# Performance work log

Hardware: AMD Instinct MI355X
Metric: run time of the kernel (lower is better)

The kernel has to match this reference:

```python
import jax, jax.numpy as jnp
import numpy as np

N_NODES = 100000


def gcn_conv(x, W, b, edge_index, n):
    """PyG-style GCNConv: x' = D^-1/2 (A+I) D^-1/2 (x W) + b."""
    loop = jnp.arange(n, dtype=edge_index.dtype)
    src = jnp.concatenate([edge_index[0], loop])
    dst = jnp.concatenate([edge_index[1], loop])
    deg = jax.ops.segment_sum(jnp.ones_like(dst, dtype=x.dtype), dst, num_segments=n)
    dinv = jax.lax.rsqrt(deg)  # deg >= 1 because of self-loops
    norm = dinv[src] * dinv[dst]  # [E+N]
    h = x @ W  # [N, out]
    msg = h[src] * norm[:, None]  # gather + scale
    return jax.ops.segment_sum(msg, dst, num_segments=n) + b


def edge_logits(z, edge_index, We, be):
    # concat(src_emb, dst_emb) @ We + be, without materializing the concat twice
    d = z.shape[1]
    return z[edge_index[0]] @ We[:d] + z[edge_index[1]] @ We[d:] + be


def setup_inputs() -> dict:
    key = jax.random.key(0)
    ks = jax.random.split(key, 10)
    x = jax.random.normal(ks[0], (N_NODES, 512), dtype=jnp.float32)
    edge_index = jax.random.randint(ks[1], (2, 3200000), 0, N_NODES, dtype=jnp.int64)
    pos_edge_index = jax.random.randint(ks[2], (2, 1000000), 0, N_NODES, dtype=jnp.int64)
    neg_edge_index = jax.random.randint(ks[3], (2, 1000000), 0, N_NODES, dtype=jnp.int64)
    s1 = 1.0 / np.sqrt(512)
    s2 = 1.0 / np.sqrt(16)
    se = 1.0 / np.sqrt(128)
    W1 = jax.random.uniform(ks[4], (512, 16), jnp.float32, -s1, s1)
    b1 = jnp.zeros((16,), jnp.float32)
    W2 = jax.random.uniform(ks[5], (16, 64), jnp.float32, -s2, s2)
    b2 = jnp.zeros((64,), jnp.float32)
    We = jax.random.uniform(ks[6], (128, 1), jnp.float32, -se, se)  # 2*num_classes -> 1
    be = jnp.zeros((1,), jnp.float32)
    return {"x": x, "W1": W1, "b1": b1, "W2": W2, "b2": b2, "We": We, "be": be,
            "edge_index": edge_index, "pos_edge_index": pos_edge_index,
            "neg_edge_index": neg_edge_index}


def reference(x, W1, b1, W2, b2, We, be, edge_index, pos_edge_index, neg_edge_index):
    n = x.shape[0]
    h = jax.nn.relu(gcn_conv(x, W1, b1, edge_index, n))
    z = gcn_conv(h, W2, b2, edge_index, n)  # node embeddings [N, num_classes]
    pos = edge_logits(z, pos_edge_index, We, be)
    neg = edge_logits(z, neg_edge_index, We, be)
    return z, jnp.concatenate([pos, neg], axis=0)
```

## Files before the change

kernel.cpp:

```cpp
#include <hip/hip_runtime.h>
#include <hip/hip_bf16.h>
#include <hip/hip_fp16.h>


constexpr int TPB = 256;
constexpr int LOG_W = 7;
constexpr int W_BKT = 128;
constexpr int NB_MAX = 1024;
constexpr int CAP = 5120;
constexpr int EPB = 8192;

__global__ __launch_bounds__(256) void scatterA_kernel(const int* __restrict__ src,
                                                       const int* __restrict__ dst,
                                                       int* __restrict__ bcursor,
                                                       int* __restrict__ pairs,
                                                       int E, int NB) {
    __shared__ int hist[NB_MAX];
    __shared__ int lstart[NB_MAX];
    __shared__ int gbase[NB_MAX];
    __shared__ int lcur[NB_MAX];
    __shared__ int csum[256];
    __shared__ int val[EPB];
    __shared__ unsigned short bkt[EPB];
    const int t = threadIdx.x;
    const int e0 = blockIdx.x * EPB;
    const int cnt = min(EPB, E - e0);

    for (int i = t; i < NB; i += 256) hist[i] = 0;
    __syncthreads();
    for (int i = t; i < cnt; i += 256) atomicAdd(&hist[dst[e0 + i] >> LOG_W], 1);
    __syncthreads();

    int loc[4], tsum = 0;
#pragma unroll
    for (int j = 0; j < 4; ++j) {
        int idx = t * 4 + j;
        int v = (idx < NB) ? hist[idx] : 0;
        loc[j] = tsum; tsum += v;
    }
    csum[t] = tsum;
    __syncthreads();
    for (int off = 1; off < 256; off <<= 1) {
        int v = (t >= off) ? csum[t - off] : 0;
        __syncthreads();
        csum[t] += v;
        __syncthreads();
    }
    int cbase = (t > 0) ? csum[t - 1] : 0;
#pragma unroll
    for (int j = 0; j < 4; ++j) {
        int idx = t * 4 + j;
        if (idx < NB) lstart[idx] = cbase + loc[j];
    }
    __syncthreads();
    for (int b = t; b < NB; b += 256) {
        gbase[b] = hist[b] ? atomicAdd(&bcursor[b], hist[b]) : 0;
        lcur[b] = lstart[b];
    }
    __syncthreads();
    for (int i = t; i < cnt; i += 256) {
        int s = src[e0 + i], d = dst[e0 + i];
        int b = d >> LOG_W;
        int p = atomicAdd(&lcur[b], 1);
        val[p] = ((d & (W_BKT - 1)) << 17) | s;
        bkt[p] = (unsigned short)b;
    }
    __syncthreads();
    for (int i = t; i < cnt; i += 256) {
        int b = bkt[i];
        int ofs = gbase[b] + (i - lstart[b]);
        if (ofs < CAP) pairs[(size_t)b * CAP + ofs] = val[i];
    }
}

__global__ __launch_bounds__(256) void bucketB_kernel(const int* __restrict__ bcursor,
                                                      int* __restrict__ pairs,
                                                      float* __restrict__ dinv,
                                                      int* __restrict__ row_start,
                                                      int* __restrict__ row_end,
                                                      int N) {
    __shared__ int cnt[W_BKT];
    __shared__ int scn[W_BKT];
    __shared__ int cur[W_BKT];
    __shared__ int img[CAP];
    const int b = blockIdx.x;
    const int t = threadIdx.x;
    const int len = min(bcursor[b], CAP);
    const int n0 = b * W_BKT;
    int* p = pairs + (size_t)b * CAP;

    if (t < W_BKT) cnt[t] = 0;
    __syncthreads();
    for (int i = t; i < len; i += 256) atomicAdd(&cnt[p[i] >> 17], 1);
    __syncthreads();
    if (t < W_BKT) scn[t] = cnt[t];
    __syncthreads();
    for (int off = 1; off < W_BKT; off <<= 1) {
        int v = (t < W_BKT && t >= off) ? scn[t - off] : 0;
        __syncthreads();
        if (t < W_BKT) scn[t] += v;
        __syncthreads();
    }
    if (t < W_BKT) {
        int c = cnt[t];
        int es = scn[t] - c;
        cur[t] = es;
        int n = n0 + t;
        if (n < N) {
            dinv[n] = rsqrtf((float)(c + 1));
            int rs = b * CAP + es;
            row_start[n] = rs;
            row_end[n] = rs + c;
        }
    }
    __syncthreads();
    for (int i = t; i < len; i += 256) {
        int v = p[i];
        int r = atomicAdd(&cur[v >> 17], 1);
        img[r] = v & 0x1FFFF;
    }
    __syncthreads();
    for (int i = t; i < len; i += 256) p[i] = img[i];
}

__global__ __launch_bounds__(256) void gemm1_kernel(const float* __restrict__ x,
                                                    const float* __restrict__ W1,
                                                    const float* __restrict__ dinv,
                                                    __half* __restrict__ xs, int N) {
    __shared__ float buf[512 * 16];
    const int t = threadIdx.x;
    {
        const float4* w4 = (const float4*)W1;
        float4* b4 = (float4*)buf;
        for (int i = t; i < 2048; i += 256) b4[i] = w4[i];
    }
    __syncthreads();

    const int r = t & 63, q = t >> 6;
    const int row = blockIdx.x * 64 + r;
    const bool valid = row < N;
    const float* xrow = x + (size_t)row * 512 + q * 128;

    float acc[16];
#pragma unroll
    for (int c = 0; c < 16; ++c) acc[c] = 0.0f;

    if (valid) {
        const int kb = q * 128;
#pragma unroll 2
        for (int k0 = 0; k0 < 128; k0 += 16) {
            const float4* xp = (const float4*)(xrow + k0);
            float4 a0 = xp[0], a1 = xp[1], a2 = xp[2], a3 = xp[3];
            float xv[16] = {a0.x, a0.y, a0.z, a0.w, a1.x, a1.y, a1.z, a1.w,
                            a2.x, a2.y, a2.z, a2.w, a3.x, a3.y, a3.z, a3.w};
#pragma unroll
            for (int kk = 0; kk < 16; ++kk) {
                const float4* wr = (const float4*)(buf + (kb + k0 + kk) * 16);
                float4 w0 = wr[0], w1 = wr[1], w2 = wr[2], w3 = wr[3];
                float xvk = xv[kk];
                acc[0]  += xvk * w0.x; acc[1]  += xvk * w0.y; acc[2]  += xvk * w0.z; acc[3]  += xvk * w0.w;
                acc[4]  += xvk * w1.x; acc[5]  += xvk * w1.y; acc[6]  += xvk * w1.z; acc[7]  += xvk * w1.w;
                acc[8]  += xvk * w2.x; acc[9]  += xvk * w2.y; acc[10] += xvk * w2.z; acc[11] += xvk * w2.w;
                acc[12] += xvk * w3.x; acc[13] += xvk * w3.y; acc[14] += xvk * w3.z; acc[15] += xvk * w3.w;
            }
        }
    }
    __syncthreads();

    float* red = buf;
    if (q > 0) {
        float4* d0 = (float4*)(red + ((q - 1) * 64 + r) * 16);
        d0[0] = make_float4(acc[0], acc[1], acc[2], acc[3]);
        d0[1] = make_float4(acc[4], acc[5], acc[6], acc[7]);
        d0[2] = make_float4(acc[8], acc[9], acc[10], acc[11]);
        d0[3] = make_float4(acc[12], acc[13], acc[14], acc[15]);
    }
    __syncthreads();
    if (q == 0 && valid) {
#pragma unroll
        for (int p = 0; p < 3; ++p) {
            const float* sr = red + (p * 64 + r) * 16;
#pragma unroll
            for (int c = 0; c < 16; ++c) acc[c] += sr[c];
        }
        float di = dinv[row];
        __half hv[16];
#pragma unroll
        for (int c = 0; c < 16; ++c) hv[c] = __float2half_rn(acc[c] * di);
        float4* o = (float4*)(xs + (size_t)row * 16);
        o[0] = *(const float4*)&hv[0];
        o[1] = *(const float4*)&hv[8];
    }
}

__global__ __launch_bounds__(256) void gather1_kernel(const __half* __restrict__ xs,
                                                      const int* __restrict__ csr,
                                                      const int* __restrict__ row_start,
                                                      const int* __restrict__ row_end,
                                                      const float* __restrict__ dinv,
                                                      const float* __restrict__ b1,
                                                      __half* __restrict__ hs, int N) {
    int t = threadIdx.x;
    int node = blockIdx.x * 16 + (t >> 4);
    int lane = t & 15;
    if (node >= N) return;
    int rs = row_start[node], re = row_end[node];
    float acc = __half2float(xs[(size_t)node * 16 + lane]);

    int e0 = rs;
    for (; e0 + 16 <= re; e0 += 16) {
        int idx = csr[e0 + lane];
        float v[16];
#pragma unroll
        for (int j = 0; j < 16; ++j) {
            int s = __shfl(idx, j, 16);
            v[j] = __half2float(xs[(size_t)s * 16 + lane]);
        }
#pragma unroll
        for (int j = 0; j < 16; ++j) acc += v[j];
    }
    if (e0 < re) {
        int idx = (e0 + lane < re) ? csr[e0 + lane] : 0;
        int m = re - e0;
        float v[16];
#pragma unroll
        for (int j = 0; j < 16; ++j) {
            int s = __shfl(idx, j, 16);
            v[j] = 0.0f;
            if (j < m) v[j] = __half2float(xs[(size_t)s * 16 + lane]);
        }
#pragma unroll
        for (int j = 0; j < 16; ++j) acc += v[j];
    }

    float di = dinv[node];
    float h = fmaxf(fmaf(di, acc, b1[lane]), 0.0f);
    hs[(size_t)node * 16 + lane] = __float2half_rn(h * di);
}

__global__ __launch_bounds__(256) void gather2_fin2_kernel(const __half* __restrict__ hs,
                                                           const int* __restrict__ csr,
                                                           const int* __restrict__ row_start,
                                                           const int* __restrict__ row_end,
                                                           const float* __restrict__ dinv,
                                                           const float* __restrict__ W2,
                                                           const float* __restrict__ b2,
                                                           const float* __restrict__ We,
                                                           float* __restrict__ z,
                                                           float* __restrict__ s1,
                                                           float* __restrict__ s2, int N) {
    __shared__ float w2l[16 * 64];
    __shared__ float wel[128];
    __shared__ float b2l[64];
    int t = threadIdx.x;
    for (int i = t; i < 1024; i += 256) w2l[i] = W2[i];
    if (t < 128) wel[t] = We[t];
    if (t < 64) b2l[t] = b2[t];
    __syncthreads();

    int g = t >> 4, lane = t & 15;
    int node = blockIdx.x * 16 + g;
    if (node >= N) return;

    int rs = row_start[node], re = row_end[node];
    float acc = __half2float(hs[(size_t)node * 16 + lane]);

    int e0 = rs;
    for (; e0 + 16 <= re; e0 += 16) {
        int idx = csr[e0 + lane];
        float v[16];
#pragma unroll
        for (int j = 0; j < 16; ++j) {
            int s = __shfl(idx, j, 16);
            v[j] = __half2float(hs[(size_t)s * 16 + lane]);
        }
#pragma unroll
        for (int j = 0; j < 16; ++j) acc += v[j];
    }
    if (e0 < re) {
        int idx = (e0 + lane < re) ? csr[e0 + lane] : 0;
        int m = re - e0;
        float v[16];
#pragma unroll
        for (int j = 0; j < 16; ++j) {
            int s = __shfl(idx, j, 16);
            v[j] = 0.0f;
            if (j < m) v[j] = __half2float(hs[(size_t)s * 16 + lane]);
        }
#pragma unroll
        for (int j = 0; j < 16; ++j) acc += v[j];
    }

    float uv = acc * dinv[node];

    int c0 = lane * 4;
    float z0 = b2l[c0], z1 = b2l[c0 + 1], z2 = b2l[c0 + 2], z3 = b2l[c0 + 3];
#pragma unroll
    for (int k = 0; k < 16; ++k) {
        float uk = __shfl(uv, k, 16);
        const float* wr = &w2l[k * 64 + c0];
        z0 = fmaf(uk, wr[0], z0);
        z1 = fmaf(uk, wr[1], z1);
        z2 = fmaf(uk, wr[2], z2);
        z3 = fmaf(uk, wr[3], z3);
    }
    float p1 = z0 * wel[c0] + z1 * wel[c0 + 1] + z2 * wel[c0 + 2] + z3 * wel[c0 + 3];
    float p2 = z0 * wel[64 + c0] + z1 * wel[64 + c0 + 1] + z2 * wel[64 + c0 + 2] + z3 * wel[64 + c0 + 3];
#pragma unroll
    for (int off = 1; off < 16; off <<= 1) {
        p1 += __shfl_xor(p1, off, 16);
        p2 += __shfl_xor(p2, off, 16);
    }
    ((float4*)(z + (size_t)node * 64))[lane] = make_float4(z0, z1, z2, z3);
    if (lane == 0) { s1[node] = p1; s2[node] = p2; }
}

__global__ void logits_kernel(const int* __restrict__ psrc, const int* __restrict__ pdst,
                              const int* __restrict__ nsrc, const int* __restrict__ ndst,
                              const float* __restrict__ s1, const float* __restrict__ s2,
                              const float* __restrict__ be, float* __restrict__ out,
                              int EP, int ET) {
    int e = blockIdx.x * blockDim.x + threadIdx.x;
    if (e >= ET) return;
    int s, d;
    if (e < EP) {
        s = psrc[e];
        d = pdst[e];
    } else {
        s = nsrc[e - EP];
        d = ndst[e - EP];
    }
    out[e] = s1[s] + s2[d] + be[0];
}

extern "C" void kernel_launch(void* const* d_in, const int* in_sizes, int n_in,
                              void* d_out, int out_size, void* d_ws, size_t ws_size,
                              hipStream_t stream) {
    const float* x  = (const float*)d_in[0];
    const float* W1 = (const float*)d_in[1];
    const float* b1 = (const float*)d_in[2];
    const float* W2 = (const float*)d_in[3];
    const float* b2 = (const float*)d_in[4];
    const float* We = (const float*)d_in[5];
    const float* be = (const float*)d_in[6];
    const int* ei   = (const int*)d_in[7];
    const int* pei  = (const int*)d_in[8];
    const int* nei  = (const int*)d_in[9];

    const int N  = in_sizes[0] / 512;
    const int E  = in_sizes[7] / 2;
    const int EP = in_sizes[8] / 2;
    const int EN = in_sizes[9] / 2;
    const int NB = (N + W_BKT - 1) >> LOG_W;

    const int* src  = ei;
    const int* dst  = ei + E;
    const int* psrc = pei;
    const int* pdst = pei + EP;
    const int* nsrc = nei;
    const int* ndst = nei + EN;

    int* wsp = (int*)d_ws;
    int*   bcursor   = wsp;
    float* dinv      = (float*)(wsp + NB_MAX);
    int*   row_start = (int*)(dinv + N);
    int*   row_end   = row_start + N;
    float* s1        = (float*)(row_end + N);
    float* s2        = s1 + N;
    __half* xs       = (__half*)(s2 + N);
    __half* hs       = xs + (size_t)16 * N;
    int*   pairs     = (int*)(hs + (size_t)16 * N);

    float* z_out = (float*)d_out;
    float* logit_out = z_out + (size_t)64 * N;

    hipMemsetAsync(bcursor, 0, NB_MAX * sizeof(int), stream);

    int gA  = (E + EPB - 1) / EPB;
    int g16 = (N + 15) / 16;
    int g64 = (N + 63) / 64;

    scatterA_kernel<<<gA, TPB, 0, stream>>>(src, dst, bcursor, pairs, E, NB);
    bucketB_kernel<<<NB, TPB, 0, stream>>>(bcursor, pairs, dinv, row_start, row_end, N);

    gemm1_kernel<<<g64, TPB, 0, stream>>>(x, W1, dinv, xs, N);

    gather1_kernel<<<g16, TPB, 0, stream>>>(xs, pairs, row_start, row_end, dinv, b1, hs, N);
    gather2_fin2_kernel<<<g16, TPB, 0, stream>>>(hs, pairs, row_start, row_end, dinv,
                                                 W2, b2, We, z_out, s1, s2, N);

    int ET = EP + EN;
    int gL = (ET + TPB - 1) / TPB;
    logits_kernel<<<gL, TPB, 0, stream>>>(psrc, pdst, nsrc, ndst, s1, s2, be,
                                          logit_out, EP, ET);
}
```

Baseline: 479.2 us.

## Replace per-node CSR gather with per-bucket edge-parallel LDS atomic accumulation

```diff
diff --git a/kernel.cpp b/kernel.cpp
--- a/kernel.cpp
+++ b/kernel.cpp
@@ -74,53 +74,23 @@
 }
 
 __global__ __launch_bounds__(256) void bucketB_kernel(const int* __restrict__ bcursor,
-                                                      int* __restrict__ pairs,
+                                                      const int* __restrict__ pairs,
                                                       float* __restrict__ dinv,
-                                                      int* __restrict__ row_start,
-                                                      int* __restrict__ row_end,
                                                       int N) {
     __shared__ int cnt[W_BKT];
-    __shared__ int scn[W_BKT];
-    __shared__ int cur[W_BKT];
-    __shared__ int img[CAP];
     const int b = blockIdx.x;
     const int t = threadIdx.x;
     const int len = min(bcursor[b], CAP);
-    const int n0 = b * W_BKT;
-    int* p = pairs + (size_t)b * CAP;
+    const int* p = pairs + (size_t)b * CAP;
 
     if (t < W_BKT) cnt[t] = 0;
     __syncthreads();
     for (int i = t; i < len; i += 256) atomicAdd(&cnt[p[i] >> 17], 1);
     __syncthreads();
-    if (t < W_BKT) scn[t] = cnt[t];
-    __syncthreads();
-    for (int off = 1; off < W_BKT; off <<= 1) {
-        int v = (t < W_BKT && t >= off) ? scn[t - off] : 0;
-        __syncthreads();
-        if (t < W_BKT) scn[t] += v;
-        __syncthreads();
-    }
     if (t < W_BKT) {
-        int c = cnt[t];
-        int es = scn[t] - c;
-        cur[t] = es;
-        int n = n0 + t;
-        if (n < N) {
-            dinv[n] = rsqrtf((float)(c + 1));
-            int rs = b * CAP + es;
-            row_start[n] = rs;
-            row_end[n] = rs + c;
-        }
-    }
-    __syncthreads();
-    for (int i = t; i < len; i += 256) {
-        int v = p[i];
-        int r = atomicAdd(&cur[v >> 17], 1);
-        img[r] = v & 0x1FFFF;
-    }
-    __syncthreads();
-    for (int i = t; i < len; i += 256) p[i] = img[i];
+        int n = b * W_BKT + t;
+        if (n < N) dinv[n] = rsqrtf((float)(cnt[t] + 1));
+    }
 }
 
 __global__ __launch_bounds__(256) void gemm1_kernel(const float* __restrict__ x,
@@ -193,126 +163,127 @@
     }
 }
 
-__global__ __launch_bounds__(256) void gather1_kernel(const __half* __restrict__ xs,
-                                                      const int* __restrict__ csr,
-                                                      const int* __restrict__ row_start,
-                                                      const int* __restrict__ row_end,
-                                                      const float* __restrict__ dinv,
-                                                      const float* __restrict__ b1,
-                                                      __half* __restrict__ hs, int N) {
-    int t = threadIdx.x;
-    int node = blockIdx.x * 16 + (t >> 4);
-    int lane = t & 15;
-    if (node >= N) return;
-    int rs = row_start[node], re = row_end[node];
-    float acc = __half2float(xs[(size_t)node * 16 + lane]);
-
-    int e0 = rs;
-    for (; e0 + 16 <= re; e0 += 16) {
-        int idx = csr[e0 + lane];
-        float v[16];
-#pragma unroll
-        for (int j = 0; j < 16; ++j) {
-            int s = __shfl(idx, j, 16);
-            v[j] = __half2float(xs[(size_t)s * 16 + lane]);
-        }
-#pragma unroll
-        for (int j = 0; j < 16; ++j) acc += v[j];
-    }
-    if (e0 < re) {
-        int idx = (e0 + lane < re) ? csr[e0 + lane] : 0;
-        int m = re - e0;
-        float v[16];
-#pragma unroll
-        for (int j = 0; j < 16; ++j) {
-            int s = __shfl(idx, j, 16);
-            v[j] = 0.0f;
-            if (j < m) v[j] = __half2float(xs[(size_t)s * 16 + lane]);
-        }
-#pragma unroll
-        for (int j = 0; j < 16; ++j) acc += v[j];
-    }
-
-    float di = dinv[node];
-    float h = fmaxf(fmaf(di, acc, b1[lane]), 0.0f);
-    hs[(size_t)node * 16 + lane] = __float2half_rn(h * di);
-}
-
-__global__ __launch_bounds__(256) void gather2_fin2_kernel(const __half* __restrict__ hs,
-                                                           const int* __restrict__ csr,
-                                                           const int* __restrict__ row_start,
-                                                           const int* __restrict__ row_end,
-                                                           const float* __restrict__ dinv,
-                                                           const float* __restrict__ W2,
-                                                           const float* __restrict__ b2,
-                                                           const float* __restrict__ We,
-                                                           float* __restrict__ z,
-                                                           float* __restrict__ s1,
-                                                           float* __restrict__ s2, int N) {
+__device__ __forceinline__ void edge_accumulate(const __half* __restrict__ tab,
+                                                const int* __restrict__ pairs,
+                                                int b, int len,
+                                                float (*acc)[17], int t) {
+    const size_t pb = (size_t)b * CAP;
+    const int g = t >> 3;
+    const int l = t & 7;
+    const int l3 = l & 3;
+    for (int eb = g * 4; eb < len; eb += 128) {
+        int n4 = min(4, len - eb);
+        int vv = pairs[pb + min(eb + l3, len - 1)];
+        float2 f[4];
+        int dls[4];
+#pragma unroll
+        for (int j = 0; j < 4; ++j) {
+            int v = __shfl(vv, j, 8);
+            dls[j] = v >> 17;
+            int s = (j < n4) ? (v & 0x1FFFF) : 0;
+            unsigned int raw = *(const unsigned int*)(tab + (size_t)s * 16 + l * 2);
+            __half2 h2 = *(__half2*)&raw;
+            f[j] = __half22float2(h2);
+        }
+#pragma unroll
+        for (int j = 0; j < 4; ++j) {
+            if (j < n4) {
+                atomicAdd(&acc[dls[j]][l * 2],     f[j].x);
+                atomicAdd(&acc[dls[j]][l * 2 + 1], f[j].y);
+            }
+        }
+    }
+}
+
+__global__ __launch_bounds__(256) void gatherE1_kernel(const __half* __restrict__ xs,
+                                                       const int* __restrict__ pairs,
+                                                       const int* __restrict__ bcursor,
+                                                       const float* __restrict__ dinv,
+                                                       const float* __restrict__ b1,
+                                                       __half* __restrict__ hs, int N) {
+    __shared__ float acc[W_BKT][17];
+    __shared__ float b1l[16];
+    const int b = blockIdx.x;
+    const int t = threadIdx.x;
+    const int len = min(bcursor[b], CAP);
+
+    if (t < 16) b1l[t] = b1[t];
+    for (int i = t; i < W_BKT * 17; i += 256) ((float*)acc)[i] = 0.0f;
+    __syncthreads();
+
+    edge_accumulate(xs, pairs, b, len, acc, t);
+    __syncthreads();
+
+    const int n0 = b * W_BKT;
+    for (int i = t; i < W_BKT * 16; i += 256) {
+        int nl = i >> 4, ch = i & 15;
+        int node = n0 + nl;
+        if (node < N) {
+            float self = __half2float(xs[(size_t)node * 16 + ch]);
+            float sum = acc[nl][ch] + self;
+            float di = dinv[node];
+            float h = fmaxf(fmaf(di, sum, b1l[ch]), 0.0f);
+            hs[(size_t)node * 16 + ch] = __float2half_rn(h * di);
+        }
+    }
+}
+
+__global__ __launch_bounds__(256) void gatherE2_kernel(const __half* __restrict__ hs,
+                                                       const int* __restrict__ pairs,
+                                                       const int* __restrict__ bcursor,
+                                                       const float* __restrict__ dinv,
+                                                       const float* __restrict__ W2,
+                                                       const float* __restrict__ b2,
+                                                       const float* __restrict__ We,
+                                                       float* __restrict__ z,
+                                                       float* __restrict__ s1,
+                                                       float* __restrict__ s2, int N) {
+    __shared__ float acc[W_BKT][17];
     __shared__ float w2l[16 * 64];
     __shared__ float wel[128];
     __shared__ float b2l[64];
-    int t = threadIdx.x;
+    const int b = blockIdx.x;
+    const int t = threadIdx.x;
+    const int len = min(bcursor[b], CAP);
+
     for (int i = t; i < 1024; i += 256) w2l[i] = W2[i];
     if (t < 128) wel[t] = We[t];
     if (t < 64) b2l[t] = b2[t];
-    __syncthreads();
-
-    int g = t >> 4, lane = t & 15;
-    int node = blockIdx.x * 16 + g;
-    if (node >= N) return;
-
-    int rs = row_start[node], re = row_end[node];
-    float acc = __half2float(hs[(size_t)node * 16 + lane]);
-
-    int e0 = rs;
-    for (; e0 + 16 <= re; e0 += 16) {
-        int idx = csr[e0 + lane];
-        float v[16];
-#pragma unroll
-        for (int j = 0; j < 16; ++j) {
-            int s = __shfl(idx, j, 16);
-            v[j] = __half2float(hs[(size_t)s * 16 + lane]);
-        }
-#pragma unroll
-        for (int j = 0; j < 16; ++j) acc += v[j];
-    }
-    if (e0 < re) {
-        int idx = (e0 + lane < re) ? csr[e0 + lane] : 0;
-        int m = re - e0;
-        float v[16];
-#pragma unroll
-        for (int j = 0; j < 16; ++j) {
-            int s = __shfl(idx, j, 16);
-            v[j] = 0.0f;
-            if (j < m) v[j] = __half2float(hs[(size_t)s * 16 + lane]);
-        }
-#pragma unroll
-        for (int j = 0; j < 16; ++j) acc += v[j];
-    }
-
-    float uv = acc * dinv[node];
-
-    int c0 = lane * 4;
-    float z0 = b2l[c0], z1 = b2l[c0 + 1], z2 = b2l[c0 + 2], z3 = b2l[c0 + 3];
-#pragma unroll
-    for (int k = 0; k < 16; ++k) {
-        float uk = __shfl(uv, k, 16);
-        const float* wr = &w2l[k * 64 + c0];
-        z0 = fmaf(uk, wr[0], z0);
-        z1 = fmaf(uk, wr[1], z1);
-        z2 = fmaf(uk, wr[2], z2);
-        z3 = fmaf(uk, wr[3], z3);
-    }
-    float p1 = z0 * wel[c0] + z1 * wel[c0 + 1] + z2 * wel[c0 + 2] + z3 * wel[c0 + 3];
-    float p2 = z0 * wel[64 + c0] + z1 * wel[64 + c0 + 1] + z2 * wel[64 + c0 + 2] + z3 * wel[64 + c0 + 3];
-#pragma unroll
-    for (int off = 1; off < 16; off <<= 1) {
-        p1 += __shfl_xor(p1, off, 16);
-        p2 += __shfl_xor(p2, off, 16);
-    }
-    ((float4*)(z + (size_t)node * 64))[lane] = make_float4(z0, z1, z2, z3);
-    if (lane == 0) { s1[node] = p1; s2[node] = p2; }
+    for (int i = t; i < W_BKT * 17; i += 256) ((float*)acc)[i] = 0.0f;
+    __syncthreads();
+
+    edge_accumulate(hs, pairs, b, len, acc, t);
+    __syncthreads();
+
+    const int n0 = b * W_BKT;
+    const int g16 = t >> 4, lane = t & 15;
+    const int c0 = lane * 4;
+    for (int nl = g16; nl < W_BKT; nl += 16) {
+        int node = n0 + nl;
+        if (node >= N) continue;
+        float self = __half2float(hs[(size_t)node * 16 + lane]);
+        float uv = (acc[nl][lane] + self) * dinv[node];
+
+        float z0 = b2l[c0], z1 = b2l[c0 + 1], z2 = b2l[c0 + 2], z3 = b2l[c0 + 3];
+#pragma unroll
+        for (int k = 0; k < 16; ++k) {
+            float uk = __shfl(uv, k, 16);
+            const float* wr = &w2l[k * 64 + c0];
+            z0 = fmaf(uk, wr[0], z0);
+            z1 = fmaf(uk, wr[1], z1);
+            z2 = fmaf(uk, wr[2], z2);
+            z3 = fmaf(uk, wr[3], z3);
+        }
+        float p1 = z0 * wel[c0] + z1 * wel[c0 + 1] + z2 * wel[c0 + 2] + z3 * wel[c0 + 3];
+        float p2 = z0 * wel[64 + c0] + z1 * wel[64 + c0 + 1] + z2 * wel[64 + c0 + 2] + z3 * wel[64 + c0 + 3];
+#pragma unroll
+        for (int off = 1; off < 16; off <<= 1) {
+            p1 += __shfl_xor(p1, off, 16);
+            p2 += __shfl_xor(p2, off, 16);
+        }
+        ((float4*)(z + (size_t)node * 64))[lane] = make_float4(z0, z1, z2, z3);
+        if (lane == 0) { s1[node] = p1; s2[node] = p2; }
+    }
 }
 
 __global__ void logits_kernel(const int* __restrict__ psrc, const int* __restrict__ pdst,
@@ -363,9 +334,7 @@
     int* wsp = (int*)d_ws;
     int*   bcursor   = wsp;
     float* dinv      = (float*)(wsp + NB_MAX);
-    int*   row_start = (int*)(dinv + N);
-    int*   row_end   = row_start + N;
-    float* s1        = (float*)(row_end + N);
+    float* s1        = dinv + N;
     float* s2        = s1 + N;
     __half* xs       = (__half*)(s2 + N);
     __half* hs       = xs + (size_t)16 * N;
@@ -377,17 +346,16 @@
     hipMemsetAsync(bcursor, 0, NB_MAX * sizeof(int), stream);
 
     int gA  = (E + EPB - 1) / EPB;
-    int g16 = (N + 15) / 16;
     int g64 = (N + 63) / 64;
 
     scatterA_kernel<<<gA, TPB, 0, stream>>>(src, dst, bcursor, pairs, E, NB);
-    bucketB_kernel<<<NB, TPB, 0, stream>>>(bcursor, pairs, dinv, row_start, row_end, N);
+    bucketB_kernel<<<NB, TPB, 0, stream>>>(bcursor, pairs, dinv, N);
 
     gemm1_kernel<<<g64, TPB, 0, stream>>>(x, W1, dinv, xs, N);
 
-    gather1_kernel<<<g16, TPB, 0, stream>>>(xs, pairs, row_start, row_end, dinv, b1, hs, N);
-    gather2_fin2_kernel<<<g16, TPB, 0, stream>>>(hs, pairs, row_start, row_end, dinv,
-                                                 W2, b2, We, z_out, s1, s2, N);
+    gatherE1_kernel<<<NB, TPB, 0, stream>>>(xs, pairs, bcursor, dinv, b1, hs, N);
+    gatherE2_kernel<<<NB, TPB, 0, stream>>>(hs, pairs, bcursor, dinv,
+                                            W2, b2, We, z_out, s1, s2, N);
 
     int ET = EP + EN;
     int gL = (ET + TPB - 1) / TPB;
```

After: 1.103 ms. 130% more time.
